# Optimization experiments

Hardware: AMD Instinct MI355X
Metric: run time of the kernel (lower is better)

The kernel has to match this reference:

```python
import jax, jax.numpy as jnp
import numpy as np

B, S, DM = 2, 2048, 1024  # batch, seq_len, model_dim
H, HD = 16, 64            # num_heads, head_dim (H*HD == DM)


def setup_inputs() -> dict:
    key = jax.random.key(0)
    ks = jax.random.split(key, 8)
    scale = 0.02
    return {
        "k": jax.random.normal(ks[0], (B, S, DM), jnp.float32),
        "q": jax.random.normal(ks[1], (B, S, DM), jnp.float32),
        "v": jax.random.normal(ks[2], (B, S, DM), jnp.float32),
        "Wk": jax.random.normal(ks[3], (DM, H * HD), jnp.float32) * scale,
        "bk": jnp.zeros((H * HD,), jnp.float32),
        "Wq": jax.random.normal(ks[4], (DM, H * HD), jnp.float32) * scale,
        "bq": jnp.zeros((H * HD,), jnp.float32),
        "Wv": jax.random.normal(ks[5], (DM, H * HD), jnp.float32) * scale,
        "bv": jnp.zeros((H * HD,), jnp.float32),
        "Wo": jax.random.normal(ks[6], (H * HD, DM), jnp.float32) * scale,
        "bo": jnp.zeros((DM,), jnp.float32),
    }


def reference(k, q, v, Wk, bk, Wq, bq, Wv, bv, Wo, bo):
    # QKV projections (Dense with bias)
    kp = (k @ Wk + bk).reshape(B, S, H, HD)
    qp = (q @ Wq + bq).reshape(B, S, H, HD)
    vp = (v @ Wv + bv).reshape(B, S, H, HD)
    # Faithful to original: scores indexed [b, key_c, h, query_q],
    # softmax over the QUERY axis, NO 1/sqrt(head_dim) scaling.
    scores = jnp.einsum('bchd,bqhd->bchq', kp, qp)
    attn = jax.nn.softmax(scores, axis=-1)
    out = jnp.einsum('bchq,bqhd->bchd', attn, vp)  # [B, S(keys), H, HD]
    out = out.reshape(B, S, H * HD)
    return out @ Wo + bo
```

## Files before the change

kernel.cpp:

```cpp
#include <hip/hip_runtime.h>
#include <hip/hip_bf16.h>
#include <stdint.h>
#include <stddef.h>


typedef __attribute__((ext_vector_type(4))) float f32x4;
typedef __attribute__((ext_vector_type(16))) float f32x16;
typedef __attribute__((ext_vector_type(8))) short s16x8;
typedef __attribute__((ext_vector_type(4))) unsigned int u32x4;
typedef __attribute__((ext_vector_type(4))) unsigned short u16x4;

#define DEV static __device__ __forceinline__

DEV unsigned short f2bf(float x) {
  unsigned int u = __float_as_uint(x);
  u += 0x7FFF + ((u >> 16) & 1);
  return (unsigned short)(u >> 16);
}
DEV f32x4 mfma16(s16x8 a, s16x8 b, f32x4 c) {
  return __builtin_amdgcn_mfma_f32_16x16x32_bf16(a, b, c, 0, 0, 0);
}
DEV f32x16 mfma32(s16x8 a, s16x8 b, f32x16 c) {
  return __builtin_amdgcn_mfma_f32_32x32x16_bf16(a, b, c, 0, 0, 0);
}
DEV f32x4 fzero() { f32x4 z; z[0]=0.f; z[1]=0.f; z[2]=0.f; z[3]=0.f; return z; }
DEV f32x16 fzero16() {
  f32x16 z;
#pragma unroll
  for (int i = 0; i < 16; ++i) z[i] = 0.f;
  return z;
}
DEV float fexp2(float x) { return __builtin_amdgcn_exp2f(x); }

DEV void gload_lds16(const unsigned short* g, unsigned short* l) {
  __builtin_amdgcn_global_load_lds(
      (const __attribute__((address_space(1))) unsigned int*)g,
      (__attribute__((address_space(3))) unsigned int*)l, 16, 0, 0);
}

#define CVTPK(dst, a, b) \
  asm("v_cvt_pk_bf16_f32 %0, %1, %2" : "=v"(dst) : "v"(a), "v"(b))
#define PSWAP(x, y) \
  asm("v_permlane32_swap_b32 %0, %1" : "+v"(x), "+v"(y))

struct CvtArgs { const float* x[3]; unsigned short* y[3]; };

__global__ __launch_bounds__(256) void cvt_kernel(CvtArgs a) {
  const float* x = a.x[blockIdx.y];
  unsigned short* y = a.y[blockIdx.y];
  const int i = blockIdx.x * 256 + threadIdx.x;
  f32x4 v = ((const f32x4*)x)[i];
  u16x4 o;
#pragma unroll
  for (int j = 0; j < 4; ++j) o[j] = f2bf(v[j]);
  ((u16x4*)y)[i] = o;
}

struct WArgs { const float* W[4]; unsigned short* Wt[4]; };

__global__ __launch_bounds__(256) void wtrans_kernel(WArgs a) {
  const float* W = a.W[blockIdx.z];
  unsigned short* Wt = a.Wt[blockIdx.z];
  const int n0 = blockIdx.x * 32, k0 = blockIdx.y * 32;
  __shared__ float t[32][33];
  const int tx = threadIdx.x & 31, ty = threadIdx.x >> 5;
#pragma unroll
  for (int i = 0; i < 4; ++i)
    t[ty + i*8][tx] = W[(size_t)(k0 + ty + i*8) * 1024 + n0 + tx];
  __syncthreads();
#pragma unroll
  for (int i = 0; i < 4; ++i)
    Wt[(size_t)(n0 + ty + i*8) * 1024 + k0 + tx] = f2bf(t[tx][ty + i*8]);
}

struct GemArgs {
  const unsigned short* A[3];
  const unsigned short* Wt[3];
  const float* bias[3];
  void* C[3];
  int mode[3];
  float scale[3];
};

template<int BM>
__global__ __launch_bounds__(256) void gemm_kernel(GemArgs g) {
  constexpr int MF = BM / 32;
  const int z = blockIdx.z;
  const unsigned short* A  = g.A[z];
  const unsigned short* Wt = g.Wt[z];
  const float* bias = g.bias[z];
  const int mode = g.mode[z];
  const float scale = g.scale[z];
  const int m0 = blockIdx.y * BM, n0 = blockIdx.x * 128;
  const int tid = threadIdx.x;
  const int lane = tid & 63, w = tid >> 6;
  const int wm = w >> 1, wn = w & 1;
  const int lg = lane >> 4, lr = lane & 15, lx = lr & 7;

  __shared__ __align__(16) unsigned short As[BM * 64];
  __shared__ __align__(16) unsigned short Bs[128 * 64];

  f32x4 acc[MF][4];
#pragma unroll
  for (int i = 0; i < MF; ++i)
#pragma unroll
    for (int j = 0; j < 4; ++j) acc[i][j] = fzero();

  const int aStep = (mode == 2) ? 2048 * 64 : 64;
  const unsigned short* srcA[MF]; unsigned short* dstA[MF];
#pragma unroll
  for (int c = 0; c < MF; ++c) {
    int n = c*256 + tid, row = n >> 3, cg = (n & 7) ^ (row & 7);
    int s = m0 + row;
    size_t abase = (mode == 2)
        ? ((size_t)((s >> 11) * 16) * 2048 + (s & 2047)) * 64 + cg * 8
        : (size_t)s * 1024 + cg * 8;
    srcA[c] = A + abase;
    dstA[c] = &As[n * 8];
  }
  const unsigned short* srcB[4]; unsigned short* dstB[4];
#pragma unroll
  for (int c = 0; c < 4; ++c) {
    int n = c*256 + tid, row = n >> 3, cg = (n & 7) ^ (row & 7);
    srcB[c] = Wt + (size_t)(n0 + row) * 1024 + cg * 8;
    dstB[c] = &Bs[n * 8];
  }

  for (int it = 0; it < 16; ++it) {
    __syncthreads();
#pragma unroll
    for (int c = 0; c < MF; ++c) { gload_lds16(srcA[c], dstA[c]); srcA[c] += aStep; }
#pragma unroll
    for (int c = 0; c < 4; ++c)  { gload_lds16(srcB[c], dstB[c]); srcB[c] += 64; }
    __syncthreads();

    s16x8 af[2][MF], bf[2][4];
#pragma unroll
    for (int ks = 0; ks < 2; ++ks) {
#pragma unroll
      for (int mf = 0; mf < MF; ++mf) {
        int row = wm*(BM/2) + mf*16 + lr;
        af[ks][mf] = *(const s16x8*)&As[row*64 + ((ks*4 + lg) ^ lx) * 8];
      }
#pragma unroll
      for (int nf = 0; nf < 4; ++nf) {
        int row = wn*64 + nf*16 + lr;
        bf[ks][nf] = *(const s16x8*)&Bs[row*64 + ((ks*4 + lg) ^ lx) * 8];
      }
    }
#pragma unroll
    for (int mf = 0; mf < MF; ++mf)
#pragma unroll
      for (int nf = 0; nf < 4; ++nf) {
        acc[mf][nf] = mfma16(af[0][mf], bf[0][nf], acc[mf][nf]);
        acc[mf][nf] = mfma16(af[1][mf], bf[1][nf], acc[mf][nf]);
      }
  }

#pragma unroll
  for (int nf = 0; nf < 4; ++nf) {
    const int colg = n0 + wn*64 + nf*16 + lr;
    const float bi = bias[colg];
#pragma unroll
    for (int mf = 0; mf < MF; ++mf) {
      const int rowg0 = m0 + wm*(BM/2) + mf*16 + lg*4;
      if (mode == 0) {
        unsigned short* o = (unsigned short*)g.C[z];
#pragma unroll
        for (int r = 0; r < 4; ++r)
          o[(size_t)(rowg0 + r) * 1024 + colg] = f2bf((acc[mf][nf][r] + bi) * scale);
      } else if (mode == 1) {
        const int hh = colg >> 6, d = colg & 63;
        const int bb2 = rowg0 >> 11, s = rowg0 & 2047;
        u16x4 pk;
#pragma unroll
        for (int r = 0; r < 4; ++r) pk[r] = f2bf(acc[mf][nf][r] + bi);
        *(u16x4*)((unsigned short*)g.C[z] + ((size_t)((bb2*16 + hh)*64 + d)) * 2048 + s) = pk;
      } else {
        float* o = (float*)g.C[z];
#pragma unroll
        for (int r = 0; r < 4; ++r)
          o[(size_t)(rowg0 + r) * 1024 + colg] = acc[mf][nf][r] + bi;
      }
    }
  }
}

__global__ __launch_bounds__(256) void attn_kernel(
    const unsigned short* __restrict__ kp, const unsigned short* __restrict__ qp,
    const unsigned short* __restrict__ vpt, unsigned short* __restrict__ aout) {
  const int F = blockIdx.x;
  const int swz = (F & 7) * 64 + (F >> 3);
  const int bh = swz >> 4, cblk = swz & 15;
  const int b = bh >> 4, h = bh & 15;
  const int c0 = cblk * 128;
  const int tid = threadIdx.x, lane = tid & 63, w = tid >> 6;
  const int cg = w & 1, jg = w >> 1;
  const int ln = lane & 31, hh = lane >> 5;

  __shared__ __align__(16) unsigned short qa_lds[2][2][2048];
  __shared__ __align__(16) unsigned short vb_lds[2][2][2048];
  __shared__ float lbuf[2][2][64];

  const int srow = tid >> 3, sp = tid & 7, sl = sp ^ (srow & 7);
  const unsigned short* qsrc0 =
      qp + (size_t)(b*2048 + srow) * 1024 + h*64 + sl*8;
  const unsigned short* qsrc1 = qsrc0 + (size_t)1024 * 1024;
  const int sd = srow + 32*(sl >> 2), sjc = sl & 3;
  const unsigned short* vsrc0 =
      vpt + ((size_t)((b*16 + h)*64) + sd) * 2048 + sjc*8;
  const unsigned short* vsrc1 = vsrc0 + 1024;

  s16x8 kbA[4], kbB[4];
  {
    const unsigned short* krowA =
        kp + (size_t)(b*2048 + c0 + cg*64 + ln) * 1024 + h*64 + hh*8;
    const unsigned short* krowB = krowA + 32 * 1024;
#pragma unroll
    for (int s = 0; s < 4; ++s) {
      kbA[s] = *(const s16x8*)(krowA + s*16);
      kbB[s] = *(const s16x8*)(krowB + s*16);
    }
  }

  f32x16 accA0 = fzero16(), accA1 = fzero16();
  f32x16 accB0 = fzero16(), accB1 = fzero16();
  float lA = 0.f, lB = 0.f;

  gload_lds16(qsrc0, &qa_lds[0][0][tid*8]);
  gload_lds16(qsrc1, &qa_lds[0][1][tid*8]);
  gload_lds16(vsrc0, &vb_lds[0][0][tid*8]);
  gload_lds16(vsrc1, &vb_lds[0][1][tid*8]);
  qsrc0 += 32*1024; qsrc1 += 32*1024; vsrc0 += 32; vsrc1 += 32;
  __syncthreads();

  for (int jt = 0; jt < 32; ++jt) {
    const int cur = jt & 1;
    if (jt + 1 < 32) {
      gload_lds16(qsrc0, &qa_lds[cur^1][0][tid*8]);
      gload_lds16(qsrc1, &qa_lds[cur^1][1][tid*8]);
      gload_lds16(vsrc0, &vb_lds[cur^1][0][tid*8]);
      gload_lds16(vsrc1, &vb_lds[cur^1][1][tid*8]);
      qsrc0 += 32*1024; qsrc1 += 32*1024; vsrc0 += 32; vsrc1 += 32;
    }

    s16x8 qa0, qa1, qa2, qa3;
    {
      const unsigned short* base = &qa_lds[cur][jg][0];
      qa0 = *(const s16x8*)&base[(ln*8 + ((0 + hh) ^ (ln & 7)))*8];
      qa1 = *(const s16x8*)&base[(ln*8 + ((2 + hh) ^ (ln & 7)))*8];
      qa2 = *(const s16x8*)&base[(ln*8 + ((4 + hh) ^ (ln & 7)))*8];
      qa3 = *(const s16x8*)&base[(ln*8 + ((6 + hh) ^ (ln & 7)))*8];
    }
    s16x8 vb0, vb1, vb2, vb3;
    {
      const unsigned short* base = &vb_lds[cur][jg][0];
      vb0 = *(const s16x8*)&base[(ln*8 + ((0 + hh) ^ (ln & 7)))*8];
      vb1 = *(const s16x8*)&base[(ln*8 + ((2 + hh) ^ (ln & 7)))*8];
      vb2 = *(const s16x8*)&base[(ln*8 + ((4 + hh) ^ (ln & 7)))*8];
      vb3 = *(const s16x8*)&base[(ln*8 + ((6 + hh) ^ (ln & 7)))*8];
    }

    f32x16 scA = fzero16(), scB = fzero16();
    __builtin_amdgcn_s_setprio(1);
    scA = mfma32(qa0, kbA[0], scA); scA = mfma32(qa1, kbA[1], scA);
    scA = mfma32(qa2, kbA[2], scA); scA = mfma32(qa3, kbA[3], scA);
    scB = mfma32(qa0, kbB[0], scB); scB = mfma32(qa1, kbB[1], scB);
    scB = mfma32(qa2, kbB[2], scB); scB = mfma32(qa3, kbB[3], scB);
    __builtin_amdgcn_s_setprio(0);

#define SOFTMAX_PV(SC, LRUN, ACC0, ACC1)                                      \
  {                                                                           \
    _Pragma("unroll")                                                         \
    for (int r = 0; r < 16; ++r) SC[r] = fexp2(SC[r]);                        \
    {                                                                         \
      float t0 = (SC[0] + SC[1]) + (SC[2] + SC[3]);                           \
      float t1 = (SC[4] + SC[5]) + (SC[6] + SC[7]);                           \
      float t2 = (SC[8] + SC[9]) + (SC[10] + SC[11]);                         \
      float t3 = (SC[12] + SC[13]) + (SC[14] + SC[15]);                       \
      LRUN += (t0 + t1) + (t2 + t3);                                          \
    }                                                                         \
    unsigned int a0, a1, b0, b1;                                              \
    u32x4 wv; s16x8 pa0, pa1;                                                 \
    CVTPK(a0, SC[0], SC[1]);  CVTPK(b0, SC[4], SC[5]);  PSWAP(a0, b0);        \
    CVTPK(a1, SC[2], SC[3]);  CVTPK(b1, SC[6], SC[7]);  PSWAP(a1, b1);        \
    wv[0] = a0; wv[1] = a1; wv[2] = b0; wv[3] = b1;                           \
    pa0 = __builtin_bit_cast(s16x8, wv);                                      \
    CVTPK(a0, SC[8], SC[9]);  CVTPK(b0, SC[12], SC[13]); PSWAP(a0, b0);       \
    CVTPK(a1, SC[10], SC[11]); CVTPK(b1, SC[14], SC[15]); PSWAP(a1, b1);      \
    wv[0] = a0; wv[1] = a1; wv[2] = b0; wv[3] = b1;                           \
    pa1 = __builtin_bit_cast(s16x8, wv);                                      \
    __builtin_amdgcn_s_setprio(1);                                            \
    ACC0 = mfma32(vb0, pa0, ACC0);                                            \
    ACC0 = mfma32(vb1, pa1, ACC0);                                            \
    ACC1 = mfma32(vb2, pa0, ACC1);                                            \
    ACC1 = mfma32(vb3, pa1, ACC1);                                            \
    __builtin_amdgcn_s_setprio(0);                                            \
  }

    SOFTMAX_PV(scA, lA, accA0, accA1);
    SOFTMAX_PV(scB, lB, accB0, accB1);
#undef SOFTMAX_PV

    __syncthreads();
  }

  float* mrg = cg ? (float*)&vb_lds[0][0][0] : (float*)&qa_lds[0][0][0];
  if (jg == 1) {
    lbuf[cg][0][lane] = lA; lbuf[cg][1][lane] = lB;
#pragma unroll
    for (int r = 0; r < 16; ++r) {
      mrg[(r)*64 + lane]      = accA0[r];
      mrg[(16 + r)*64 + lane] = accA1[r];
      mrg[(32 + r)*64 + lane] = accB0[r];
      mrg[(48 + r)*64 + lane] = accB1[r];
    }
  }
  __syncthreads();
  if (jg == 0) {
    lA += lbuf[cg][0][lane]; lB += lbuf[cg][1][lane];
#pragma unroll
    for (int r = 0; r < 16; ++r) {
      accA0[r] += mrg[(r)*64 + lane];
      accA1[r] += mrg[(16 + r)*64 + lane];
      accB0[r] += mrg[(32 + r)*64 + lane];
      accB1[r] += mrg[(48 + r)*64 + lane];
    }
    lA += __shfl_xor(lA, 32);
    lB += __shfl_xor(lB, 32);
    const float invA = 1.0f / lA, invB = 1.0f / lB;
    unsigned short* obaseA =
        aout + ((size_t)bh * 2048 + c0 + cg*64 + ln) * 64 + hh * 4;
    unsigned short* obaseB = obaseA + 32 * 64;
#pragma unroll
    for (int dt = 0; dt < 2; ++dt)
#pragma unroll
      for (int rq = 0; rq < 4; ++rq) {
        u16x4 pkA, pkB;
#pragma unroll
        for (int i = 0; i < 4; ++i) {
          const int reg = rq*4 + i;
          pkA[i] = f2bf(((dt == 0) ? accA0[reg] : accA1[reg]) * invA);
          pkB[i] = f2bf(((dt == 0) ? accB0[reg] : accB1[reg]) * invB);
        }
        *(u16x4*)(obaseA + dt*32 + rq*8) = pkA;
        *(u16x4*)(obaseB + dt*32 + rq*8) = pkB;
      }
  }
}

extern "C" void kernel_launch(void* const* d_in, const int* in_sizes, int n_in,
                              void* d_out, int out_size, void* d_ws, size_t ws_size,
                              hipStream_t stream) {
  (void)in_sizes; (void)n_in; (void)out_size; (void)ws_size;
  const float* k  = (const float*)d_in[0];
  const float* q  = (const float*)d_in[1];
  const float* v  = (const float*)d_in[2];
  const float* Wk = (const float*)d_in[3];
  const float* bk = (const float*)d_in[4];
  const float* Wq = (const float*)d_in[5];
  const float* bq = (const float*)d_in[6];
  const float* Wv = (const float*)d_in[7];
  const float* bv = (const float*)d_in[8];
  const float* Wo = (const float*)d_in[9];
  const float* bo = (const float*)d_in[10];

  char* ws = (char*)d_ws;
  const size_t MB = 1024 * 1024;
  unsigned short* Wkt = (unsigned short*)(ws + 0*MB);
  unsigned short* Wqt = (unsigned short*)(ws + 2*MB);
  unsigned short* Wvt = (unsigned short*)(ws + 4*MB);
  unsigned short* Wot = (unsigned short*)(ws + 6*MB);
  unsigned short* kp  = (unsigned short*)(ws + 8*MB);
  unsigned short* qp  = (unsigned short*)(ws + 16*MB);
  unsigned short* vpt = (unsigned short*)(ws + 24*MB);
  unsigned short* vc  = (unsigned short*)(ws + 32*MB);
  unsigned short* aoutb = (unsigned short*)(ws + 40*MB);
  unsigned short* kc = (unsigned short*)d_out;
  unsigned short* qc = (unsigned short*)((char*)d_out + 8*MB);

  CvtArgs ca;
  ca.x[0] = k; ca.x[1] = q; ca.x[2] = v;
  ca.y[0] = kc; ca.y[1] = qc; ca.y[2] = vc;
  cvt_kernel<<<dim3(4096, 3), 256, 0, stream>>>(ca);

  WArgs wa;
  wa.W[0] = Wk; wa.W[1] = Wq; wa.W[2] = Wv; wa.W[3] = Wo;
  wa.Wt[0] = Wkt; wa.Wt[1] = Wqt; wa.Wt[2] = Wvt; wa.Wt[3] = Wot;
  wtrans_kernel<<<dim3(32, 32, 4), 256, 0, stream>>>(wa);

  GemArgs gp;
  gp.A[0] = kc; gp.A[1] = qc; gp.A[2] = vc;
  gp.Wt[0] = Wkt; gp.Wt[1] = Wqt; gp.Wt[2] = Wvt;
  gp.bias[0] = bk; gp.bias[1] = bq; gp.bias[2] = bv;
  gp.C[0] = kp; gp.C[1] = qp; gp.C[2] = vpt;
  gp.mode[0] = 0; gp.mode[1] = 0; gp.mode[2] = 1;
  gp.scale[0] = 1.4426950408889634f;
  gp.scale[1] = 1.0f; gp.scale[2] = 1.0f;
  gemm_kernel<128><<<dim3(8, 32, 3), 256, 0, stream>>>(gp);

  attn_kernel<<<dim3(512), 256, 0, stream>>>(kp, qp, vpt, aoutb);

  GemArgs gf;
  gf.A[0] = aoutb; gf.A[1] = aoutb; gf.A[2] = aoutb;
  gf.Wt[0] = Wot; gf.Wt[1] = Wot; gf.Wt[2] = Wot;
  gf.bias[0] = bo; gf.bias[1] = bo; gf.bias[2] = bo;
  gf.C[0] = d_out; gf.C[1] = d_out; gf.C[2] = d_out;
  gf.mode[0] = 2; gf.mode[1] = 2; gf.mode[2] = 2;
  gf.scale[0] = 1.0f; gf.scale[1] = 1.0f; gf.scale[2] = 1.0f;
  gemm_kernel<64><<<dim3(8, 64, 1), 256, 0, stream>>>(gf);
}
```

Baseline: 135.0 us.

## Merge prep kernels, swizzle GEMM block order, compute softmax row sums via MFMA

Folds the activation-to-bf16 conversion and the weight transpose into one launch, with each conversion thread now handling eight elements. GEMM blocks are remapped in groups of eight so that neighbouring blocks share tiles in cache. In attention, the per-row exp sums are computed by an extra MFMA against a ones vector, replacing the scalar adds and the cross-lane shuffle. The extra MFMAs add matrix-core work per tile, and bf16-rounded probabilities in the sum change numerics slightly.

Result: faster. 125.3 us (-7.1%).

```diff
diff --git a/kernel.cpp b/kernel.cpp
--- a/kernel.cpp
+++ b/kernel.cpp
@@ -43,34 +43,39 @@
 #define PSWAP(x, y) \
   asm("v_permlane32_swap_b32 %0, %1" : "+v"(x), "+v"(y))
 
-struct CvtArgs { const float* x[3]; unsigned short* y[3]; };
-
-__global__ __launch_bounds__(256) void cvt_kernel(CvtArgs a) {
-  const float* x = a.x[blockIdx.y];
-  unsigned short* y = a.y[blockIdx.y];
-  const int i = blockIdx.x * 256 + threadIdx.x;
-  f32x4 v = ((const f32x4*)x)[i];
-  u16x4 o;
-#pragma unroll
-  for (int j = 0; j < 4; ++j) o[j] = f2bf(v[j]);
-  ((u16x4*)y)[i] = o;
-}
-
-struct WArgs { const float* W[4]; unsigned short* Wt[4]; };
-
-__global__ __launch_bounds__(256) void wtrans_kernel(WArgs a) {
-  const float* W = a.W[blockIdx.z];
-  unsigned short* Wt = a.Wt[blockIdx.z];
-  const int n0 = blockIdx.x * 32, k0 = blockIdx.y * 32;
+struct PrepArgs {
+  const float* x[3]; unsigned short* y[3];
+  const float* W[4]; unsigned short* Wt[4];
+};
+
+__global__ __launch_bounds__(256) void prep_kernel(PrepArgs a) {
   __shared__ float t[32][33];
-  const int tx = threadIdx.x & 31, ty = threadIdx.x >> 5;
-#pragma unroll
-  for (int i = 0; i < 4; ++i)
-    t[ty + i*8][tx] = W[(size_t)(k0 + ty + i*8) * 1024 + n0 + tx];
-  __syncthreads();
-#pragma unroll
-  for (int i = 0; i < 4; ++i)
-    Wt[(size_t)(n0 + ty + i*8) * 1024 + k0 + tx] = f2bf(t[tx][ty + i*8]);
+  const int plane = blockIdx.y;
+  if (plane < 3) {
+    const float* x = a.x[plane];
+    unsigned short* y = a.y[plane];
+    const int i = blockIdx.x * 256 + threadIdx.x;
+    f32x4 v0 = ((const f32x4*)x)[2*i];
+    f32x4 v1 = ((const f32x4*)x)[2*i + 1];
+    u16x4 o0, o1;
+#pragma unroll
+    for (int j = 0; j < 4; ++j) { o0[j] = f2bf(v0[j]); o1[j] = f2bf(v1[j]); }
+    ((u16x4*)y)[2*i] = o0;
+    ((u16x4*)y)[2*i + 1] = o1;
+  } else {
+    if (blockIdx.x >= 1024) return;
+    const float* W = a.W[plane - 3];
+    unsigned short* Wt = a.Wt[plane - 3];
+    const int n0 = (blockIdx.x & 31) * 32, k0 = (blockIdx.x >> 5) * 32;
+    const int tx = threadIdx.x & 31, ty = threadIdx.x >> 5;
+#pragma unroll
+    for (int i = 0; i < 4; ++i)
+      t[ty + i*8][tx] = W[(size_t)(k0 + ty + i*8) * 1024 + n0 + tx];
+    __syncthreads();
+#pragma unroll
+    for (int i = 0; i < 4; ++i)
+      Wt[(size_t)(n0 + ty + i*8) * 1024 + k0 + tx] = f2bf(t[tx][ty + i*8]);
+  }
 }
 
 struct GemArgs {
@@ -91,7 +96,11 @@
   const float* bias = g.bias[z];
   const int mode = g.mode[z];
   const float scale = g.scale[z];
-  const int m0 = blockIdx.y * BM, n0 = blockIdx.x * 128;
+  const int Fb = blockIdx.y * gridDim.x + blockIdx.x;
+  const int chunk = gridDim.y >> 3;
+  const int myi = (Fb & 7) * chunk + ((Fb >> 3) % chunk);
+  const int nxi = (Fb >> 3) / chunk;
+  const int m0 = myi * BM, n0 = nxi * 128;
   const int tid = threadIdx.x;
   const int lane = tid & 63, w = tid >> 6;
   const int wm = w >> 1, wn = w & 1;
@@ -223,9 +232,17 @@
     }
   }
 
+  s16x8 onesA, onesB;
+  {
+    const short oa = (short)((ln < 16) ? 0x3F80 : 0);
+    const short ob = (short)((ln < 16) ? 0 : 0x3F80);
+#pragma unroll
+    for (int i = 0; i < 8; ++i) { onesA[i] = oa; onesB[i] = ob; }
+  }
+
   f32x16 accA0 = fzero16(), accA1 = fzero16();
   f32x16 accB0 = fzero16(), accB1 = fzero16();
-  float lA = 0.f, lB = 0.f;
+  f32x16 lacc = fzero16();
 
   gload_lds16(qsrc0, &qa_lds[0][0][tid*8]);
   gload_lds16(qsrc1, &qa_lds[0][1][tid*8]);
@@ -269,17 +286,10 @@
     scB = mfma32(qa2, kbB[2], scB); scB = mfma32(qa3, kbB[3], scB);
     __builtin_amdgcn_s_setprio(0);
 
-#define SOFTMAX_PV(SC, LRUN, ACC0, ACC1)                                      \
+#define SOFTMAX_PV(SC, ONES, ACC0, ACC1)                                      \
   {                                                                           \
     _Pragma("unroll")                                                         \
     for (int r = 0; r < 16; ++r) SC[r] = fexp2(SC[r]);                        \
-    {                                                                         \
-      float t0 = (SC[0] + SC[1]) + (SC[2] + SC[3]);                           \
-      float t1 = (SC[4] + SC[5]) + (SC[6] + SC[7]);                           \
-      float t2 = (SC[8] + SC[9]) + (SC[10] + SC[11]);                         \
-      float t3 = (SC[12] + SC[13]) + (SC[14] + SC[15]);                       \
-      LRUN += (t0 + t1) + (t2 + t3);                                          \
-    }                                                                         \
     unsigned int a0, a1, b0, b1;                                              \
     u32x4 wv; s16x8 pa0, pa1;                                                 \
     CVTPK(a0, SC[0], SC[1]);  CVTPK(b0, SC[4], SC[5]);  PSWAP(a0, b0);        \
@@ -291,6 +301,8 @@
     wv[0] = a0; wv[1] = a1; wv[2] = b0; wv[3] = b1;                           \
     pa1 = __builtin_bit_cast(s16x8, wv);                                      \
     __builtin_amdgcn_s_setprio(1);                                            \
+    lacc = mfma32(ONES, pa0, lacc);                                           \
+    lacc = mfma32(ONES, pa1, lacc);                                           \
     ACC0 = mfma32(vb0, pa0, ACC0);                                            \
     ACC0 = mfma32(vb1, pa1, ACC0);                                            \
     ACC1 = mfma32(vb2, pa0, ACC1);                                            \
@@ -298,12 +310,14 @@
     __builtin_amdgcn_s_setprio(0);                                            \
   }
 
-    SOFTMAX_PV(scA, lA, accA0, accA1);
-    SOFTMAX_PV(scB, lB, accB0, accB1);
+    SOFTMAX_PV(scA, onesA, accA0, accA1);
+    SOFTMAX_PV(scB, onesB, accB0, accB1);
 #undef SOFTMAX_PV
 
     __syncthreads();
   }
+
+  float lA = lacc[0], lB = lacc[8];
 
   float* mrg = cg ? (float*)&vb_lds[0][0][0] : (float*)&qa_lds[0][0][0];
   if (jg == 1) {
@@ -326,8 +340,6 @@
       accB0[r] += mrg[(32 + r)*64 + lane];
       accB1[r] += mrg[(48 + r)*64 + lane];
     }
-    lA += __shfl_xor(lA, 32);
-    lB += __shfl_xor(lB, 32);
     const float invA = 1.0f / lA, invB = 1.0f / lB;
     unsigned short* obaseA =
         aout + ((size_t)bh * 2048 + c0 + cg*64 + ln) * 64 + hh * 4;
@@ -379,15 +391,12 @@
   unsigned short* kc = (unsigned short*)d_out;
   unsigned short* qc = (unsigned short*)((char*)d_out + 8*MB);
 
-  CvtArgs ca;
-  ca.x[0] = k; ca.x[1] = q; ca.x[2] = v;
-  ca.y[0] = kc; ca.y[1] = qc; ca.y[2] = vc;
-  cvt_kernel<<<dim3(4096, 3), 256, 0, stream>>>(ca);
-
-  WArgs wa;
-  wa.W[0] = Wk; wa.W[1] = Wq; wa.W[2] = Wv; wa.W[3] = Wo;
-  wa.Wt[0] = Wkt; wa.Wt[1] = Wqt; wa.Wt[2] = Wvt; wa.Wt[3] = Wot;
-  wtrans_kernel<<<dim3(32, 32, 4), 256, 0, stream>>>(wa);
+  PrepArgs pa;
+  pa.x[0] = k; pa.x[1] = q; pa.x[2] = v;
+  pa.y[0] = kc; pa.y[1] = qc; pa.y[2] = vc;
+  pa.W[0] = Wk; pa.W[1] = Wq; pa.W[2] = Wv; pa.W[3] = Wo;
+  pa.Wt[0] = Wkt; pa.Wt[1] = Wqt; pa.Wt[2] = Wvt; pa.Wt[3] = Wot;
+  prep_kernel<<<dim3(2048, 7), 256, 0, stream>>>(pa);
 
   GemArgs gp;
   gp.A[0] = kc; gp.A[1] = qc; gp.A[2] = vc;
```
